# Kernel optimization log

Measured on AMD Instinct MI355X. Metric: run time of the kernel, lower is better.

The kernel has to match this reference:

```python
import jax, jax.numpy as jnp
import numpy as np

KEY_DIM = 512
VAL_DIM = 512
BATCH = 32768
MEMORY_MAX_NORM = 5.0
TTT_LR_SCALE = 0.005
EPS = 1e-8


def setup_inputs() -> dict:
    key = jax.random.key(0)
    k1, k2, k3, k4, k5 = jax.random.split(key, 5)
    k = jax.random.normal(k1, (BATCH, KEY_DIM), dtype=jnp.float32)
    v = jax.random.normal(k2, (BATCH, VAL_DIM), dtype=jnp.float32)
    # memory weight init: normal(std=0.01)
    mem_w = jax.random.normal(k3, (VAL_DIM, KEY_DIM), dtype=jnp.float32) * 0.01
    # gate_proj: init is zeros/0.5; use small random weight + 0.5 bias for a
    # non-degenerate but realistic post-warmup state
    gate_w = jax.random.normal(k4, (3, KEY_DIM + VAL_DIM), dtype=jnp.float32) * 0.01
    gate_b = jnp.full((3,), 0.5, dtype=jnp.float32)
    momentum_S = jax.random.normal(k5, (VAL_DIM, KEY_DIM), dtype=jnp.float32) * 0.01
    return {"k": k, "v": v, "mem_w": mem_w, "gate_w": gate_w,
            "gate_b": gate_b, "momentum_S": momentum_S}


def _norm_clip(x, max_norm):
    n = jnp.linalg.norm(x)
    return jnp.where(n > max_norm, x * (max_norm / (n + EPS)), x)


def reference(k, v, mem_w, gate_w, gate_b, momentum_S):
    # retrieve: M(k) = k @ W^T ; loss = MSE(pred, v)
    retrieved = k @ mem_w.T                      # [B, val_dim]
    diff = retrieved - v
    loss = jnp.mean(diff * diff)

    # gates from batch-mean key/value
    kv_agg = jnp.concatenate([k.mean(0), v.mean(0)], axis=-1)  # [key+val]
    gates = jax.nn.sigmoid(kv_agg @ gate_w.T + gate_b)         # [3]
    alpha, eta, theta = gates[0], gates[1], gates[2]

    # analytic grad of MSE wrt W: 2/(B*val_dim) * (pred - v)^T @ k
    B, vd = diff.shape
    grad = (2.0 / (B * vd)) * (diff.T @ k)       # [val_dim, key_dim]
    grad_c = jnp.clip(grad, -1.0, 1.0)

    new_momentum = eta * momentum_S - TTT_LR_SCALE * theta * grad_c
    new_momentum = _norm_clip(new_momentum, MEMORY_MAX_NORM)

    new_weight = (1.0 - alpha) * mem_w + new_momentum
    new_weight = _norm_clip(new_weight, MEMORY_MAX_NORM)

    return retrieved, loss, new_weight, new_momentum, alpha, eta, theta
```

## Files before the change

### kernel.cpp

```cpp
#include <hip/hip_runtime.h>
#include <math.h>


typedef __bf16 bf16x8 __attribute__((ext_vector_type(8)));
typedef float f32x4 __attribute__((ext_vector_type(4)));
typedef float float4_t __attribute__((ext_vector_type(4)));
typedef unsigned short ushort4_t __attribute__((ext_vector_type(4)));
typedef unsigned short ushort8_t __attribute__((ext_vector_type(8)));

#define OUT_LOSS   16777216
#define OUT_W      16777217
#define OUT_MOM    17039361
#define OUT_ALPHA  17301505

#define OFF_GRAD   0u
#define OFF_CKP    1048576u
#define OFF_CVP    1572864u
#define OFF_LOSSP  2097152u
#define OFF_COLK   2105344u
#define OFF_COLV   2107392u
#define OFF_SCAL   2109440u
#define OFF_W16    2109504u
#define OFF_K16    2633792u
#define OFF_DIFF   36188224u
#define OFF_MRAW   OFF_K16
#define OFF_WRAW   (OFF_K16 + 1048576u)

__device__ __forceinline__ ushort4_t cvt4(float4_t v) {
  union { __bf16 b; unsigned short u; } c0, c1, c2, c3;
  c0.b = (__bf16)v.x; c1.b = (__bf16)v.y; c2.b = (__bf16)v.z; c3.b = (__bf16)v.w;
  ushort4_t h; h.x = c0.u; h.y = c1.u; h.z = c2.u; h.w = c3.u;
  return h;
}

__device__ __forceinline__ void gload_lds16(const unsigned short* g, unsigned short* l) {
  __builtin_amdgcn_global_load_lds(
      (const __attribute__((address_space(1))) unsigned int*)g,
      (__attribute__((address_space(3))) unsigned int*)l, 16, 0, 0);
}

__global__ __launch_bounds__(256) void k1_convert(
    const float* __restrict__ Kp, const float* __restrict__ Wp,
    unsigned short* __restrict__ k16, unsigned short* __restrict__ w16,
    float* __restrict__ colk_part, float* __restrict__ grad)
{
  __shared__ float cp[512];
  const int t = threadIdx.x;
  const int cg = t & 127;
  const int g = t >> 7;
  const int b = blockIdx.x;
  if (b < 256) {
    const int r0 = b << 7;
    float p0 = 0.f, p1 = 0.f, p2 = 0.f, p3 = 0.f;
#pragma unroll 4
    for (int rr = g; rr < 128; rr += 2) {
      const size_t off = (size_t)(r0 + rr) * 512 + (cg << 2);
      const float4_t v = *reinterpret_cast<const float4_t*>(&Kp[off]);
      *reinterpret_cast<ushort4_t*>(&k16[off]) = cvt4(v);
      p0 += v.x; p1 += v.y; p2 += v.z; p3 += v.w;
    }
    if (g == 1) {
      cp[(cg << 2) + 0] = p0; cp[(cg << 2) + 1] = p1;
      cp[(cg << 2) + 2] = p2; cp[(cg << 2) + 3] = p3;
    }
    __syncthreads();
    if (g == 0) {
      colk_part[(size_t)b * 512 + (cg << 2) + 0] = p0 + cp[(cg << 2) + 0];
      colk_part[(size_t)b * 512 + (cg << 2) + 1] = p1 + cp[(cg << 2) + 1];
      colk_part[(size_t)b * 512 + (cg << 2) + 2] = p2 + cp[(cg << 2) + 2];
      colk_part[(size_t)b * 512 + (cg << 2) + 3] = p3 + cp[(cg << 2) + 3];
    }
  } else if (b < 272) {
    const int r0 = (b - 256) << 5;
#pragma unroll 4
    for (int rr = g; rr < 32; rr += 2) {
      const size_t off = (size_t)(r0 + rr) * 512 + (cg << 2);
      const float4_t v = *reinterpret_cast<const float4_t*>(&Wp[off]);
      *reinterpret_cast<ushort4_t*>(&w16[off]) = cvt4(v);
    }
  } else {
    const int base = (b - 272) << 14;
    const float4_t z = (float4_t){0.f, 0.f, 0.f, 0.f};
#pragma unroll
    for (int j = 0; j < 16; ++j)
      *reinterpret_cast<float4_t*>(&grad[base + (j << 10) + (t << 2)]) = z;
  }
}

__global__ __launch_bounds__(256) void k2_gemm(
    const unsigned short* __restrict__ k16, const unsigned short* __restrict__ w16,
    const float* __restrict__ Vp, float* __restrict__ outp,
    unsigned short* __restrict__ diff16,
    float* __restrict__ colv_part, float* __restrict__ loss_part)
{
  __shared__ __align__(16) unsigned short As[8192];
  __shared__ __align__(16) unsigned short Bs[8192];
  __shared__ float redc[256];
  __shared__ float redl[4];

  const int t = threadIdx.x, lane = t & 63, wv = t >> 6;
  const int tile = (blockIdx.x & 7) * 128 + (blockIdx.x >> 3);
  const int rt = tile >> 2, vt = tile & 3;
  const int row0 = rt << 7, vd0 = vt << 7;

  f32x4 acc[4][4];
#pragma unroll
  for (int m = 0; m < 4; ++m)
#pragma unroll
    for (int n = 0; n < 4; ++n)
      acc[m][n] = (f32x4){0.f, 0.f, 0.f, 0.f};

  const int srow = (wv << 3) + (lane >> 3);
  const int scol = (lane & 7) << 3;
  const unsigned short* pA = k16 + (size_t)(row0 + srow) * 512 + scol;
  const unsigned short* pB = w16 + (size_t)(vd0 + srow) * 512 + scol;
  unsigned short* lA = &As[wv << 9];
  unsigned short* lB = &Bs[wv << 9];

  const int fr = lane & 15, fq = lane >> 4;
  const int wr = (wv >> 1) << 6, wc = (wv & 1) << 6;

  for (int kk0 = 0; kk0 < 512; kk0 += 64) {
#pragma unroll
    for (int i = 0; i < 4; ++i) {
      gload_lds16(pA + (i << 14) + kk0, lA + (i << 11));
      gload_lds16(pB + (i << 14) + kk0, lB + (i << 11));
    }
    __syncthreads();
#pragma unroll
    for (int kk = 0; kk < 64; kk += 32) {
      const int co = kk + (fq << 3);
      bf16x8 af[4], bfv[4];
#pragma unroll
      for (int m = 0; m < 4; ++m)
        af[m] = *reinterpret_cast<const bf16x8*>(&As[((wr + (m << 4) + fr) << 6) + co]);
#pragma unroll
      for (int n = 0; n < 4; ++n)
        bfv[n] = *reinterpret_cast<const bf16x8*>(&Bs[((wc + (n << 4) + fr) << 6) + co]);
#pragma unroll
      for (int m = 0; m < 4; ++m)
#pragma unroll
        for (int n = 0; n < 4; ++n)
          acc[m][n] = __builtin_amdgcn_mfma_f32_16x16x32_bf16(af[m], bfv[n], acc[m][n], 0, 0, 0);
    }
    __syncthreads();
  }

  float lsum = 0.f;
  float vcs[4] = {0.f, 0.f, 0.f, 0.f};
#pragma unroll
  for (int m = 0; m < 4; ++m) {
#pragma unroll
    for (int n = 0; n < 4; ++n) {
#pragma unroll
      for (int i = 0; i < 4; ++i) {
        const int gr = row0 + wr + (m << 4) + (fq << 2) + i;
        const int gc = vd0 + wc + (n << 4) + fr;
        const size_t oi = (size_t)gr * 512 + gc;
        const float rv = acc[m][n][i];
        outp[oi] = rv;
        const float vv = Vp[oi];
        const float d = rv - vv;
        lsum += d * d;
        vcs[n] += vv;
        union { __bf16 b; unsigned short u; } cd; cd.b = (__bf16)d;
        diff16[oi] = cd.u;
      }
    }
  }
#pragma unroll
  for (int o = 32; o; o >>= 1) lsum += __shfl_xor(lsum, o);
  if (lane == 0) redl[wv] = lsum;
#pragma unroll
  for (int n = 0; n < 4; ++n) {
    vcs[n] += __shfl_xor(vcs[n], 16);
    vcs[n] += __shfl_xor(vcs[n], 32);
  }
  if (fq == 0) {
#pragma unroll
    for (int n = 0; n < 4; ++n)
      redc[(wv << 6) + (n << 4) + fr] = vcs[n];
  }
  __syncthreads();
  if (t < 128) {
    const int side = t >> 6, lc = t & 63;
    colv_part[(size_t)rt * 512 + vd0 + t] =
        redc[side * 64 + lc] + redc[(side + 2) * 64 + lc];
  }
  if (t == 0)
    loss_part[tile] = redl[0] + redl[1] + redl[2] + redl[3];
}

__global__ __launch_bounds__(256) void k3_grad(
    const unsigned short* __restrict__ diff16,
    const unsigned short* __restrict__ k16,
    float* __restrict__ grad)
{
  __shared__ __align__(16) unsigned short At[2][128][40];
  __shared__ __align__(16) unsigned short Bt[2][128][40];
  const int t = threadIdx.x, lane = t & 63, wv = t >> 6;
  const int b = blockIdx.x;
  const int x = b & 7;
  const int q = b >> 3;
  const int tile = q & 15;
  const int kc = ((q >> 4) << 3) | x;
  const int vd0 = (tile & 3) << 7;
  const int kd0 = (tile >> 2) << 7;
  const size_t r0 = (size_t)kc << 10;

  f32x4 acc[4][4];
#pragma unroll
  for (int m = 0; m < 4; ++m)
#pragma unroll
    for (int n = 0; n < 4; ++n)
      acc[m][n] = (f32x4){0.f, 0.f, 0.f, 0.f};

  const int dr = t >> 3;
  const int c0 = (t & 7) << 4;
  const int wr = (wv >> 1) << 6, wc = (wv & 1) << 6;
  const int fr = lane & 15, fq = lane >> 4;
  const int swz = ((c0 >> 4) & 3) << 3;
  const int drs = dr ^ swz;

#define K3_LOAD(s, A0, A1, B0, B1) do {                                     \
    const size_t ro_ = (r0 + ((size_t)(s) << 5) + dr) << 9;                 \
    A0 = *reinterpret_cast<const ushort8_t*>(&diff16[ro_ + vd0 + c0]);      \
    A1 = *reinterpret_cast<const ushort8_t*>(&diff16[ro_ + vd0 + c0 + 8]);  \
    B0 = *reinterpret_cast<const ushort8_t*>(&k16[ro_ + kd0 + c0]);         \
    B1 = *reinterpret_cast<const ushort8_t*>(&k16[ro_ + kd0 + c0 + 8]);     \
  } while (0)

#define K3_WRITE(buf, A0, A1, B0, B1) do {                                  \
    _Pragma("unroll")                                                       \
    for (int j = 0; j < 8; ++j) {                                           \
      At[buf][c0 + j][drs] = A0[j];                                         \
      At[buf][c0 + 8 + j][drs] = A1[j];                                     \
      Bt[buf][c0 + j][drs] = B0[j];                                         \
      Bt[buf][c0 + 8 + j][drs] = B1[j];                                     \
    } } while (0)

#define K3_MFMA(buf) do {                                                   \
    bf16x8 af[4], bfv[4];                                                   \
    _Pragma("unroll")                                                       \
    for (int m = 0; m < 4; ++m) {                                           \
      const int rA = wr + (m << 4) + fr;                                    \
      af[m] = *reinterpret_cast<const bf16x8*>(                             \
          &At[buf][rA][(fq ^ ((rA >> 4) & 3)) << 3]);                       \
    }                                                                       \
    _Pragma("unroll")                                                       \
    for (int n = 0; n < 4; ++n) {                                           \
      const int rB = wc + (n << 4) + fr;                                    \
      bfv[n] = *reinterpret_cast<const bf16x8*>(                            \
          &Bt[buf][rB][(fq ^ ((rB >> 4) & 3)) << 3]);                       \
    }                                                                       \
    _Pragma("unroll")                                                       \
    for (int m = 0; m < 4; ++m)                                             \
      _Pragma("unroll")                                                     \
      for (int n = 0; n < 4; ++n)                                           \
        acc[m][n] = __builtin_amdgcn_mfma_f32_16x16x32_bf16(                \
            af[m], bfv[n], acc[m][n], 0, 0, 0);                             \
  } while (0)

#define K3_LBAR() do {                                                      \
    asm volatile("s_waitcnt lgkmcnt(0)" ::: "memory");                      \
    __builtin_amdgcn_s_barrier();                                           \
  } while (0)

  ushort8_t a0A, a1A, b0A, b1A, a0B, a1B, b0B, b1B;
  K3_LOAD(0, a0A, a1A, b0A, b1A);
  K3_WRITE(0, a0A, a1A, b0A, b1A);
  K3_LOAD(1, a0B, a1B, b0B, b1B);
  K3_LBAR();

#pragma unroll 1
  for (int it = 0; it < 15; ++it) {
    const int s = it << 1;
    K3_LOAD(s + 2, a0A, a1A, b0A, b1A);
    K3_WRITE(1, a0B, a1B, b0B, b1B);
    K3_MFMA(0);
    K3_LBAR();
    K3_LOAD(s + 3, a0B, a1B, b0B, b1B);
    K3_WRITE(0, a0A, a1A, b0A, b1A);
    K3_MFMA(1);
    K3_LBAR();
  }
  K3_WRITE(1, a0B, a1B, b0B, b1B);
  K3_MFMA(0);
  K3_LBAR();
  K3_MFMA(1);

#undef K3_LOAD
#undef K3_WRITE
#undef K3_MFMA
#undef K3_LBAR

#pragma unroll
  for (int m = 0; m < 4; ++m)
#pragma unroll
    for (int n = 0; n < 4; ++n)
#pragma unroll
      for (int i = 0; i < 4; ++i)
        atomicAdd(&grad[(size_t)(vd0 + wr + (m << 4) + (fq << 2) + i) * 512
                        + kd0 + wc + (n << 4) + fr], acc[m][n][i]);
}

__global__ __launch_bounds__(256) void c1a_redcols(
    const float* __restrict__ ckp, const float* __restrict__ cvp,
    float* __restrict__ colk, float* __restrict__ colv)
{
  __shared__ float red[8][32];
  const int t = threadIdx.x, b = blockIdx.x;
  const int mtx = b >> 4;
  const int c = ((b & 15) << 5) + (t & 31);
  const int pg = t >> 5;
  const float* src = mtx ? cvp : ckp;
  float s = 0.f;
  for (int p = pg; p < 256; p += 8) s += src[(size_t)p * 512 + c];
  red[pg][t & 31] = s;
  __syncthreads();
  if (pg == 0) {
    float tot = 0.f;
#pragma unroll
    for (int j = 0; j < 8; ++j) tot += red[j][t & 31];
    (mtx ? colv : colk)[c] = tot;
  }
}

__global__ __launch_bounds__(256) void c1b_gates(
    const float* __restrict__ gw, const float* __restrict__ gb,
    const float* __restrict__ colk, const float* __restrict__ colv,
    const float* __restrict__ lossp, float* __restrict__ scal,
    float* __restrict__ outp)
{
  __shared__ float red3[3][4];
  __shared__ float redl[4];
  const int t = threadIdx.x, lane = t & 63, wvi = t >> 6;
  float p3[3] = {0.f, 0.f, 0.f};
  for (int j = t; j < 1024; j += 256) {
    const float kv = (j < 512 ? colk[j] : colv[j - 512]) * (1.0f / 32768.0f);
    p3[0] += kv * gw[j];
    p3[1] += kv * gw[1024 + j];
    p3[2] += kv * gw[2048 + j];
  }
  float ls = lossp[t] + lossp[256 + t] + lossp[512 + t] + lossp[768 + t];
#pragma unroll
  for (int o = 32; o; o >>= 1) {
    ls += __shfl_xor(ls, o);
#pragma unroll
    for (int g = 0; g < 3; ++g) p3[g] += __shfl_xor(p3[g], o);
  }
  if (lane == 0) {
    red3[0][wvi] = p3[0]; red3[1][wvi] = p3[1]; red3[2][wvi] = p3[2];
    redl[wvi] = ls;
  }
  __syncthreads();
  if (t == 0) {
    const float s0 = red3[0][0] + red3[0][1] + red3[0][2] + red3[0][3] + gb[0];
    const float s1 = red3[1][0] + red3[1][1] + red3[1][2] + red3[1][3] + gb[1];
    const float s2 = red3[2][0] + red3[2][1] + red3[2][2] + red3[2][3] + gb[2];
    const float alpha = 1.0f / (1.0f + expf(-s0));
    const float eta   = 1.0f / (1.0f + expf(-s1));
    const float theta = 1.0f / (1.0f + expf(-s2));
    scal[1] = 0.f; scal[2] = 0.f;
    scal[3] = alpha; scal[4] = eta; scal[5] = theta;
    outp[OUT_LOSS] = (redl[0] + redl[1] + redl[2] + redl[3]) * (1.0f / 16777216.0f);
    outp[OUT_ALPHA]     = alpha;
    outp[OUT_ALPHA + 1] = eta;
    outp[OUT_ALPHA + 2] = theta;
  }
}

__device__ __forceinline__ void block_atomic_sumsq(float sq, float* target) {
  __shared__ float red[4];
#pragma unroll
  for (int o = 32; o; o >>= 1) sq += __shfl_xor(sq, o);
  if ((threadIdx.x & 63) == 0) red[threadIdx.x >> 6] = sq;
  __syncthreads();
  if (threadIdx.x == 0) atomicAdd(target, red[0] + red[1] + red[2] + red[3]);
}

__global__ __launch_bounds__(256) void c2_mom(
    const float* __restrict__ grad, const float* __restrict__ S,
    float* scal, float* __restrict__ m_raw)
{
  const float eta = scal[4];
  const float cth = 0.005f * scal[5];
  const int i = ((blockIdx.x << 8) + threadIdx.x) << 2;
  const float4_t g = *reinterpret_cast<const float4_t*>(&grad[i]);
  const float4_t s = *reinterpret_cast<const float4_t*>(&S[i]);
  float4_t m; float sq = 0.f;
#pragma unroll
  for (int j = 0; j < 4; ++j) {
    float gj = g[j] * (2.0f / 16777216.0f);
    gj = fminf(1.0f, fmaxf(-1.0f, gj));
    m[j] = eta * s[j] - cth * gj;
    sq += m[j] * m[j];
  }
  *reinterpret_cast<float4_t*>(&m_raw[i]) = m;
  block_atomic_sumsq(sq, &scal[1]);
}

__global__ __launch_bounds__(256) void c3_wt(
    const float* __restrict__ m_raw, const float* __restrict__ memw,
    float* scal, float* __restrict__ w_raw, float* __restrict__ outp)
{
  const float nm = sqrtf(scal[1]);
  const float sm = nm > 5.0f ? 5.0f / (nm + 1e-8f) : 1.0f;
  const float oma = 1.0f - scal[3];
  const int i = ((blockIdx.x << 8) + threadIdx.x) << 2;
  const float4_t mr = *reinterpret_cast<const float4_t*>(&m_raw[i]);
  const float4_t wi = *reinterpret_cast<const float4_t*>(&memw[i]);
  float4_t w; float sq = 0.f;
#pragma unroll
  for (int j = 0; j < 4; ++j) {
    const float m = mr[j] * sm;
    outp[OUT_MOM + i + j] = m;
    w[j] = oma * wi[j] + m;
    sq += w[j] * w[j];
  }
  *reinterpret_cast<float4_t*>(&w_raw[i]) = w;
  block_atomic_sumsq(sq, &scal[2]);
}

__global__ __launch_bounds__(256) void c4_wt(
    const float* __restrict__ w_raw, const float* __restrict__ scal,
    float* __restrict__ outp)
{
  const float nw = sqrtf(scal[2]);
  const float sw = nw > 5.0f ? 5.0f / (nw + 1e-8f) : 1.0f;
  const int i = ((blockIdx.x << 8) + threadIdx.x) << 2;
  const float4_t w = *reinterpret_cast<const float4_t*>(&w_raw[i]);
#pragma unroll
  for (int j = 0; j < 4; ++j)
    outp[OUT_W + i + j] = w[j] * sw;
}

extern "C" void kernel_launch(void* const* d_in, const int* in_sizes, int n_in,
                              void* d_out, int out_size, void* d_ws, size_t ws_size,
                              hipStream_t stream)
{
  const float* Kp = (const float*)d_in[0];
  const float* Vp = (const float*)d_in[1];
  const float* Wp = (const float*)d_in[2];
  const float* GW = (const float*)d_in[3];
  const float* GB = (const float*)d_in[4];
  const float* Sp = (const float*)d_in[5];
  float* outp = (float*)d_out;
  char* ws = (char*)d_ws;

  float* grad            = (float*)(ws + OFF_GRAD);
  float* colk_part       = (float*)(ws + OFF_CKP);
  float* colv_part       = (float*)(ws + OFF_CVP);
  float* loss_part       = (float*)(ws + OFF_LOSSP);
  float* colk            = (float*)(ws + OFF_COLK);
  float* colv            = (float*)(ws + OFF_COLV);
  float* scal            = (float*)(ws + OFF_SCAL);
  unsigned short* w16    = (unsigned short*)(ws + OFF_W16);
  unsigned short* k16    = (unsigned short*)(ws + OFF_K16);
  unsigned short* diff16 = (unsigned short*)(ws + OFF_DIFF);
  float* m_raw           = (float*)(ws + OFF_MRAW);
  float* w_raw           = (float*)(ws + OFF_WRAW);

  k1_convert<<<288, 256, 0, stream>>>(Kp, Wp, k16, w16, colk_part, grad);
  k2_gemm<<<1024, 256, 0, stream>>>(k16, w16, Vp, outp, diff16, colv_part, loss_part);
  k3_grad<<<512, 256, 0, stream>>>(diff16, k16, grad);
  c1a_redcols<<<32, 256, 0, stream>>>(colk_part, colv_part, colk, colv);
  c1b_gates<<<1, 256, 0, stream>>>(GW, GB, colk, colv, loss_part, scal, outp);
  c2_mom<<<256, 256, 0, stream>>>(grad, Sp, scal, m_raw);
  c3_wt<<<256, 256, 0, stream>>>(m_raw, Wp, scal, w_raw, outp);
  c4_wt<<<256, 256, 0, stream>>>(w_raw, scal, outp);
}
```

Measured before the change: 163.9 us.

## Compute clip norms algebraically from dot products and fuse tail kernels

Gate-independent dot products (S·S, S·g, g·g, W·W, W·S, W·g) are accumulated in one reduction pass, so the gates kernel can compute both clip norms analytically. The three-pass momentum/weight tail collapses into a single final elementwise kernel. The K column sums move from the convert kernel into the gradient GEMM's load path, using bf16 values, which lets the convert kernel become a wider pure cast. The trade-off is extra register pressure in the grad kernel, lower-precision column means, and possible cancellation error in the expanded norm formulas.

```diff
diff --git a/kernel.cpp b/kernel.cpp
--- a/kernel.cpp
+++ b/kernel.cpp
@@ -23,8 +23,6 @@
 #define OFF_W16    2109504u
 #define OFF_K16    2633792u
 #define OFF_DIFF   36188224u
-#define OFF_MRAW   OFF_K16
-#define OFF_WRAW   (OFF_K16 + 1048576u)
 
 __device__ __forceinline__ ushort4_t cvt4(float4_t v) {
   union { __bf16 b; unsigned short u; } c0, c1, c2, c3;
@@ -33,6 +31,10 @@
   return h;
 }
 
+__device__ __forceinline__ float bf2f(unsigned short u) {
+  return __uint_as_float(((unsigned int)u) << 16);
+}
+
 __device__ __forceinline__ void gload_lds16(const unsigned short* g, unsigned short* l) {
   __builtin_amdgcn_global_load_lds(
       (const __attribute__((address_space(1))) unsigned int*)g,
@@ -42,48 +44,32 @@
 __global__ __launch_bounds__(256) void k1_convert(
     const float* __restrict__ Kp, const float* __restrict__ Wp,
     unsigned short* __restrict__ k16, unsigned short* __restrict__ w16,
-    float* __restrict__ colk_part, float* __restrict__ grad)
-{
-  __shared__ float cp[512];
+    float* __restrict__ grad, float* __restrict__ scal)
+{
+  const int b = blockIdx.x;
   const int t = threadIdx.x;
-  const int cg = t & 127;
-  const int g = t >> 7;
-  const int b = blockIdx.x;
-  if (b < 256) {
-    const int r0 = b << 7;
-    float p0 = 0.f, p1 = 0.f, p2 = 0.f, p3 = 0.f;
-#pragma unroll 4
-    for (int rr = g; rr < 128; rr += 2) {
-      const size_t off = (size_t)(r0 + rr) * 512 + (cg << 2);
-      const float4_t v = *reinterpret_cast<const float4_t*>(&Kp[off]);
-      *reinterpret_cast<ushort4_t*>(&k16[off]) = cvt4(v);
-      p0 += v.x; p1 += v.y; p2 += v.z; p3 += v.w;
-    }
-    if (g == 1) {
-      cp[(cg << 2) + 0] = p0; cp[(cg << 2) + 1] = p1;
-      cp[(cg << 2) + 2] = p2; cp[(cg << 2) + 3] = p3;
-    }
-    __syncthreads();
-    if (g == 0) {
-      colk_part[(size_t)b * 512 + (cg << 2) + 0] = p0 + cp[(cg << 2) + 0];
-      colk_part[(size_t)b * 512 + (cg << 2) + 1] = p1 + cp[(cg << 2) + 1];
-      colk_part[(size_t)b * 512 + (cg << 2) + 2] = p2 + cp[(cg << 2) + 2];
-      colk_part[(size_t)b * 512 + (cg << 2) + 3] = p3 + cp[(cg << 2) + 3];
-    }
-  } else if (b < 272) {
-    const int r0 = (b - 256) << 5;
-#pragma unroll 4
-    for (int rr = g; rr < 32; rr += 2) {
-      const size_t off = (size_t)(r0 + rr) * 512 + (cg << 2);
-      const float4_t v = *reinterpret_cast<const float4_t*>(&Wp[off]);
-      *reinterpret_cast<ushort4_t*>(&w16[off]) = cvt4(v);
+  if (b < 1040) {
+    const float* src = (b < 1024) ? Kp : Wp;
+    unsigned short* dst = (b < 1024) ? k16 : w16;
+    const size_t base = (size_t)(b < 1024 ? b : b - 1024) * 16384;
+#pragma unroll
+    for (int j = 0; j < 8; ++j) {
+      const size_t off = base + (size_t)j * 2048 + ((size_t)t << 3);
+      const float4_t v0 = *reinterpret_cast<const float4_t*>(&src[off]);
+      const float4_t v1 = *reinterpret_cast<const float4_t*>(&src[off + 4]);
+      const ushort4_t h0 = cvt4(v0), h1 = cvt4(v1);
+      ushort8_t h;
+      h[0] = h0.x; h[1] = h0.y; h[2] = h0.z; h[3] = h0.w;
+      h[4] = h1.x; h[5] = h1.y; h[6] = h1.z; h[7] = h1.w;
+      *reinterpret_cast<ushort8_t*>(&dst[off]) = h;
     }
   } else {
-    const int base = (b - 272) << 14;
+    const int base = (b - 1040) << 14;
     const float4_t z = (float4_t){0.f, 0.f, 0.f, 0.f};
 #pragma unroll
     for (int j = 0; j < 16; ++j)
       *reinterpret_cast<float4_t*>(&grad[base + (j << 10) + (t << 2)]) = z;
+    if (b == 1040 && t < 16) scal[t] = 0.f;
   }
 }
 
@@ -194,7 +180,7 @@
 __global__ __launch_bounds__(256) void k3_grad(
     const unsigned short* __restrict__ diff16,
     const unsigned short* __restrict__ k16,
-    float* __restrict__ grad)
+    float* __restrict__ grad, float* __restrict__ colk_part)
 {
   __shared__ __align__(16) unsigned short At[2][128][40];
   __shared__ __align__(16) unsigned short Bt[2][128][40];
@@ -215,6 +201,10 @@
     for (int n = 0; n < 4; ++n)
       acc[m][n] = (f32x4){0.f, 0.f, 0.f, 0.f};
 
+  float ck[16];
+#pragma unroll
+  for (int j = 0; j < 16; ++j) ck[j] = 0.f;
+
   const int dr = t >> 3;
   const int c0 = (t & 7) << 4;
   const int wr = (wv >> 1) << 6, wc = (wv & 1) << 6;
@@ -237,6 +227,12 @@
       At[buf][c0 + 8 + j][drs] = A1[j];                                     \
       Bt[buf][c0 + j][drs] = B0[j];                                         \
       Bt[buf][c0 + 8 + j][drs] = B1[j];                                     \
+    }                                                                       \
+    if (vd0 == 0) {                                                         \
+      _Pragma("unroll")                                                     \
+      for (int j = 0; j < 8; ++j) {                                         \
+        ck[j] += bf2f(B0[j]); ck[8 + j] += bf2f(B1[j]);                     \
+      }                                                                     \
     } } while (0)
 
 #define K3_MFMA(buf) do {                                                   \
@@ -302,27 +298,87 @@
       for (int i = 0; i < 4; ++i)
         atomicAdd(&grad[(size_t)(vd0 + wr + (m << 4) + (fq << 2) + i) * 512
                         + kd0 + wc + (n << 4) + fr], acc[m][n][i]);
-}
-
-__global__ __launch_bounds__(256) void c1a_redcols(
+
+  if (vd0 == 0) {
+#pragma unroll
+    for (int j = 0; j < 16; ++j) {
+      ck[j] += __shfl_xor(ck[j], 8);
+      ck[j] += __shfl_xor(ck[j], 16);
+      ck[j] += __shfl_xor(ck[j], 32);
+    }
+    __syncthreads();
+    float* cred = (float*)&At[0][0][0];
+    if (lane < 8) {
+#pragma unroll
+      for (int j = 0; j < 16; ++j) cred[(wv << 7) + (lane << 4) + j] = ck[j];
+    }
+    __syncthreads();
+    if (t < 128) {
+      colk_part[(size_t)kc * 512 + kd0 + t] =
+          cred[t] + cred[128 + t] + cred[256 + t] + cred[384 + t];
+    }
+  }
+}
+
+__global__ __launch_bounds__(256) void cR_reduce(
     const float* __restrict__ ckp, const float* __restrict__ cvp,
-    float* __restrict__ colk, float* __restrict__ colv)
-{
-  __shared__ float red[8][32];
+    float* __restrict__ colk, float* __restrict__ colv,
+    const float* __restrict__ grad, const float* __restrict__ S,
+    const float* __restrict__ Wm, float* __restrict__ scal)
+{
   const int t = threadIdx.x, b = blockIdx.x;
-  const int mtx = b >> 4;
-  const int c = ((b & 15) << 5) + (t & 31);
-  const int pg = t >> 5;
-  const float* src = mtx ? cvp : ckp;
-  float s = 0.f;
-  for (int p = pg; p < 256; p += 8) s += src[(size_t)p * 512 + c];
-  red[pg][t & 31] = s;
-  __syncthreads();
-  if (pg == 0) {
-    float tot = 0.f;
-#pragma unroll
-    for (int j = 0; j < 8; ++j) tot += red[j][t & 31];
-    (mtx ? colv : colk)[c] = tot;
+  if (b < 32) {
+    __shared__ float red[8][32];
+    const int mtx = b >> 4;
+    const int c = ((b & 15) << 5) + (t & 31);
+    const int pg = t >> 5;
+    const float* src = mtx ? cvp : ckp;
+    const int P = mtx ? 256 : 32;
+    float s = 0.f;
+    for (int p = pg; p < P; p += 8) s += src[(size_t)p * 512 + c];
+    red[pg][t & 31] = s;
+    __syncthreads();
+    if (pg == 0) {
+      float tot = 0.f;
+#pragma unroll
+      for (int j = 0; j < 8; ++j) tot += red[j][t & 31];
+      (mtx ? colv : colk)[c] = tot;
+    }
+  } else {
+    __shared__ float red6[6][4];
+    const int qb = b - 32;
+    float d[6] = {0.f, 0.f, 0.f, 0.f, 0.f, 0.f};
+#pragma unroll
+    for (int j = 0; j < 16; ++j) {
+      const int i = (qb << 14) + (j << 10) + (t << 2);
+      const float4_t g4 = *reinterpret_cast<const float4_t*>(&grad[i]);
+      const float4_t s4 = *reinterpret_cast<const float4_t*>(&S[i]);
+      const float4_t w4 = *reinterpret_cast<const float4_t*>(&Wm[i]);
+#pragma unroll
+      for (int e = 0; e < 4; ++e) {
+        float gt = g4[e] * (2.0f / 16777216.0f);
+        gt = fminf(1.0f, fmaxf(-1.0f, gt));
+        d[0] += s4[e] * s4[e];
+        d[1] += s4[e] * gt;
+        d[2] += gt * gt;
+        d[3] += w4[e] * w4[e];
+        d[4] += w4[e] * s4[e];
+        d[5] += w4[e] * gt;
+      }
+    }
+    const int lane = t & 63, wvi = t >> 6;
+#pragma unroll
+    for (int k = 0; k < 6; ++k) {
+#pragma unroll
+      for (int o = 32; o; o >>= 1) d[k] += __shfl_xor(d[k], o);
+    }
+    if (lane == 0) {
+#pragma unroll
+      for (int k = 0; k < 6; ++k) red6[k][wvi] = d[k];
+    }
+    __syncthreads();
+    if (t < 6)
+      atomicAdd(&scal[8 + t], red6[t][0] + red6[t][1] + red6[t][2] + red6[t][3]);
   }
 }
 
@@ -361,8 +417,19 @@
     const float alpha = 1.0f / (1.0f + expf(-s0));
     const float eta   = 1.0f / (1.0f + expf(-s1));
     const float theta = 1.0f / (1.0f + expf(-s2));
-    scal[1] = 0.f; scal[2] = 0.f;
+    const float ct = 0.005f * theta;
+    const float SS = scal[8], Sg = scal[9], gg = scal[10];
+    const float WW = scal[11], WS = scal[12], Wg = scal[13];
+    const float nm2 = eta * eta * SS - 2.0f * eta * ct * Sg + ct * ct * gg;
+    const float nm = sqrtf(fmaxf(nm2, 0.f));
+    const float sm = nm > 5.0f ? 5.0f / (nm + 1e-8f) : 1.0f;
+    const float Wmred = sm * (eta * WS - ct * Wg);
+    const float oma = 1.0f - alpha;
+    const float nw2 = oma * oma * WW + 2.0f * oma * Wmred + sm * sm * nm2;
+    const float nw = sqrtf(fmaxf(nw2, 0.f));
+    const float sw = nw > 5.0f ? 5.0f / (nw + 1e-8f) : 1.0f;
     scal[3] = alpha; scal[4] = eta; scal[5] = theta;
+    scal[6] = sm; scal[7] = sw;
     outp[OUT_LOSS] = (redl[0] + redl[1] + redl[2] + redl[3]) * (1.0f / 16777216.0f);
     outp[OUT_ALPHA]     = alpha;
     outp[OUT_ALPHA + 1] = eta;
@@ -370,69 +437,27 @@
   }
 }
 
-__device__ __forceinline__ void block_atomic_sumsq(float sq, float* target) {
-  __shared__ float red[4];
-#pragma unroll
-  for (int o = 32; o; o >>= 1) sq += __shfl_xor(sq, o);
-  if ((threadIdx.x & 63) == 0) red[threadIdx.x >> 6] = sq;
-  __syncthreads();
-  if (threadIdx.x == 0) atomicAdd(target, red[0] + red[1] + red[2] + red[3]);
-}
-
-__global__ __launch_bounds__(256) void c2_mom(
+__global__ __launch_bounds__(256) void cF_final(
     const float* __restrict__ grad, const float* __restrict__ S,
-    float* scal, float* __restrict__ m_raw)
-{
-  const float eta = scal[4];
-  const float cth = 0.005f * scal[5];
+    const float* __restrict__ Wm, const float* __restrict__ scal,
+    float* __restrict__ outp)
+{
+  const float alpha = scal[3], eta = scal[4];
+  const float ct = 0.005f * scal[5];
+  const float sm = scal[6], sw = scal[7];
+  const float oma = 1.0f - alpha;
   const int i = ((blockIdx.x << 8) + threadIdx.x) << 2;
-  const float4_t g = *reinterpret_cast<const float4_t*>(&grad[i]);
-  const float4_t s = *reinterpret_cast<const float4_t*>(&S[i]);
-  float4_t m; float sq = 0.f;
+  const float4_t g4 = *reinterpret_cast<const float4_t*>(&grad[i]);
+  const float4_t s4 = *reinterpret_cast<const float4_t*>(&S[i]);
+  const float4_t w4 = *reinterpret_cast<const float4_t*>(&Wm[i]);
 #pragma unroll
   for (int j = 0; j < 4; ++j) {
-    float gj = g[j] * (2.0f / 16777216.0f);
-    gj = fminf(1.0f, fmaxf(-1.0f, gj));
-    m[j] = eta * s[j] - cth * gj;
-    sq += m[j] * m[j];
-  }
-  *reinterpret_cast<float4_t*>(&m_raw[i]) = m;
-  block_atomic_sumsq(sq, &scal[1]);
-}
-
-__global__ __launch_bounds__(256) void c3_wt(
-    const float* __restrict__ m_raw, const float* __restrict__ memw,
-    float* scal, float* __restrict__ w_raw, float* __restrict__ outp)
-{
-  const float nm = sqrtf(scal[1]);
-  const float sm = nm > 5.0f ? 5.0f / (nm + 1e-8f) : 1.0f;
-  const float oma = 1.0f - scal[3];
-  const int i = ((blockIdx.x << 8) + threadIdx.x) << 2;
-  const float4_t mr = *reinterpret_cast<const float4_t*>(&m_raw[i]);
-  const float4_t wi = *reinterpret_cast<const float4_t*>(&memw[i]);
-  float4_t w; float sq = 0.f;
-#pragma unroll
-  for (int j = 0; j < 4; ++j) {
-    const float m = mr[j] * sm;
+    float gt = g4[j] * (2.0f / 16777216.0f);
+    gt = fminf(1.0f, fmaxf(-1.0f, gt));
+    const float m = sm * (eta * s4[j] - ct * gt);
     outp[OUT_MOM + i + j] = m;
-    w[j] = oma * wi[j] + m;
-    sq += w[j] * w[j];
-  }
-  *reinterpret_cast<float4_t*>(&w_raw[i]) = w;
-  block_atomic_sumsq(sq, &scal[2]);
-}
-
-__global__ __launch_bounds__(256) void c4_wt(
-    const float* __restrict__ w_raw, const float* __restrict__ scal,
-    float* __restrict__ outp)
-{
-  const float nw = sqrtf(scal[2]);
-  const float sw = nw > 5.0f ? 5.0f / (nw + 1e-8f) : 1.0f;
-  const int i = ((blockIdx.x << 8) + threadIdx.x) << 2;
-  const float4_t w = *reinterpret_cast<const float4_t*>(&w_raw[i]);
-#pragma unroll
-  for (int j = 0; j < 4; ++j)
-    outp[OUT_W + i + j] = w[j] * sw;
+    outp[OUT_W + i + j] = sw * (oma * w4[j] + m);
+  }
 }
 
 extern "C" void kernel_launch(void* const* d_in, const int* in_sizes, int n_in,
@@ -458,15 +483,12 @@
   unsigned short* w16    = (unsigned short*)(ws + OFF_W16);
   unsigned short* k16    = (unsigned short*)(ws + OFF_K16);
   unsigned short* diff16 = (unsigned short*)(ws + OFF_DIFF);
-  float* m_raw           = (float*)(ws + OFF_MRAW);
-  float* w_raw           = (float*)(ws + OFF_WRAW);
-
-  k1_convert<<<288, 256, 0, stream>>>(Kp, Wp, k16, w16, colk_part, grad);
+
+  k1_convert<<<1056, 256, 0, stream>>>(Kp, Wp, k16, w16, grad, scal);
   k2_gemm<<<1024, 256, 0, stream>>>(k16, w16, Vp, outp, diff16, colv_part, loss_part);
-  k3_grad<<<512, 256, 0, stream>>>(diff16, k16, grad);
-  c1a_redcols<<<32, 256, 0, stream>>>(colk_part, colv_part, colk, colv);
+  k3_grad<<<512, 256, 0, stream>>>(diff16, k16, grad, colk_part);
+  cR_reduce<<<48, 256, 0, stream>>>(colk_part, colv_part, colk, colv,
+                                    grad, Sp, Wp, scal);
   c1b_gates<<<1, 256, 0, stream>>>(GW, GB, colk, colv, loss_part, scal, outp);
-  c2_mom<<<256, 256, 0, stream>>>(grad, Sp, scal, m_raw);
-  c3_wt<<<256, 256, 0, stream>>>(m_raw, Wp, scal, w_raw, outp);
-  c4_wt<<<256, 256, 0, stream>>>(w_raw, scal, outp);
-}
+  cF_final<<<256, 256, 0, stream>>>(grad, Sp, Wp, scal, outp);
+}
```

After: 150.0 us, median of 2. 1.09x faster.
